# Performance work log

Measured on AMD Instinct MI355X. Metric: run time of the kernel, lower is better.

## Reference

```python
import jax, jax.numpy as jnp
import numpy as np

L = 16            # table_num (levels)
LOG2T = 14
T = 1 << LOG2T    # entries per table
Z = 512           # z_dim
S = 256           # style_dim
IMG = 256         # img_size
RES_MIN, RES_MAX = 16, 256
HID, OUT = 64, 3  # mlp hidden / out dims
B = 8
FDIM = 2 * L      # retrieved feature dim (2 per level)
PRIME = jnp.uint32(2654435761)  # instant-ngp hash prime
GAIN = 1.4142135623730951       # stylegan lrelu gain sqrt(2)
# geometric level resolutions res_min -> res_max
RES = np.floor(RES_MIN * np.exp(np.arange(L) * np.log(RES_MAX / RES_MIN) / (L - 1))).astype(np.float32)


def _lrelu(x):
    return GAIN * jnp.where(x >= 0, x, 0.2 * x)


def _coords():
    c = (jnp.arange(IMG, dtype=jnp.float32) + 0.5) / IMG
    x, y = jnp.meshgrid(c, c, indexing='ij')
    return jnp.stack((x, y), -1).reshape(-1, 2)  # (N, 2), N = IMG*IMG


def _mod_linear(x, s, aw, ab, w, b):
    # StyleGAN2-style modulated linear with demodulation. x: (B,N,in), s: (B,S)
    style = s @ aw + ab                                   # (B, in)
    demod = jax.lax.rsqrt((style ** 2) @ (w ** 2) + 1e-8)  # (B, out)
    return ((x * style[:, None, :]) @ w) * demod[:, None, :] + b


def _forward(z, mw0, mb0, mw1, mb1, mw2, mb2, base_tables, w_mod, b_mod,
             a0w, a0b, w0, bb0, a1w, a1b, w1, bb1, a2w, a2b, w2, bb2):
    s = _lrelu(z @ mw0 + mb0)
    s = _lrelu(s @ mw1 + mb1)
    s = _lrelu(s @ mw2 + mb2)                              # (B, S)
    # style-conditioned hash tables: per-level per-channel modulation of base tables
    scale = 1.0 + (s @ w_mod + b_mod).reshape(-1, L, 1, 2)
    tables = base_tables[None] * scale                     # (B, L, T, 2)

    coords = _coords()                                     # (N, 2)
    offs = jnp.array([[0, 0], [1, 0], [0, 1], [1, 1]], dtype=jnp.uint32)
    feats = []
    for l in range(L):
        pos = coords * RES[l]
        p0 = jnp.floor(pos)
        frac = pos - p0                                    # (N, 2)
        p0i = p0.astype(jnp.uint32)
        cx = p0i[None, :, 0] + offs[:, 0:1]                # (4, N)
        cy = p0i[None, :, 1] + offs[:, 1:2]
        idx = ((cx ^ (cy * PRIME)) & jnp.uint32(T - 1)).astype(jnp.int32)  # (4, N)
        wx = jnp.where(offs[:, 0:1] == 1, frac[None, :, 0], 1.0 - frac[None, :, 0])
        wy = jnp.where(offs[:, 1:2] == 1, frac[None, :, 1], 1.0 - frac[None, :, 1])
        wgt = wx * wy                                      # (4, N)
        tl = tables[:, l]                                  # (B, T, 2)
        f = jnp.take(tl, idx.reshape(-1), axis=1).reshape(tl.shape[0], 4, -1, 2)
        feats.append(jnp.einsum('bcnd,cn->bnd', f, wgt))   # bilinear interp
    h = jnp.concatenate(feats, -1)                         # (B, N, 2L)

    # stacked modulated MLP (3 layers), final tanh, then render to image
    h = _lrelu(_mod_linear(h, s, a0w, a0b, w0, bb0))
    h = _lrelu(_mod_linear(h, s, a1w, a1b, w1, bb1))
    h = jnp.tanh(_mod_linear(h, s, a2w, a2b, w2, bb2))     # (B, N, 3)
    return h.reshape(-1, IMG, IMG, OUT).transpose(0, 3, 1, 2)


def setup_inputs() -> dict:
    key = jax.random.key(0)
    ks = jax.random.split(key, 12)
    nrm = lambda k, sh, sc: jax.random.normal(k, sh, jnp.float32) * sc
    inp = {}
    inp['z'] = jax.random.normal(ks[0], (B, Z), jnp.float32)
    inp['mw0'] = nrm(ks[1], (Z, S), 1 / np.sqrt(Z)); inp['mb0'] = jnp.zeros((S,), jnp.float32)
    inp['mw1'] = nrm(ks[2], (S, S), 1 / np.sqrt(S)); inp['mb1'] = jnp.zeros((S,), jnp.float32)
    inp['mw2'] = nrm(ks[3], (S, S), 1 / np.sqrt(S)); inp['mb2'] = jnp.zeros((S,), jnp.float32)
    inp['base_tables'] = nrm(ks[4], (L, T, 2), 0.1)
    inp['w_mod'] = nrm(ks[5], (S, L * 2), 1 / np.sqrt(S)); inp['b_mod'] = jnp.zeros((L * 2,), jnp.float32)
    inp['a0w'] = nrm(ks[6], (S, FDIM), 1 / np.sqrt(S)); inp['a0b'] = jnp.ones((FDIM,), jnp.float32)
    inp['w0'] = nrm(ks[7], (FDIM, HID), 1 / np.sqrt(FDIM)); inp['bb0'] = jnp.zeros((HID,), jnp.float32)
    inp['a1w'] = nrm(ks[8], (S, HID), 1 / np.sqrt(S)); inp['a1b'] = jnp.ones((HID,), jnp.float32)
    inp['w1'] = nrm(ks[9], (HID, HID), 1 / np.sqrt(HID)); inp['bb1'] = jnp.zeros((HID,), jnp.float32)
    inp['a2w'] = nrm(ks[10], (S, HID), 1 / np.sqrt(S)); inp['a2b'] = jnp.ones((HID,), jnp.float32)
    inp['w2'] = nrm(ks[11], (HID, OUT), 1 / np.sqrt(HID)); inp['bb2'] = jnp.zeros((OUT,), jnp.float32)
    return inp


def reference(z, mw0, mb0, mw1, mb1, mw2, mb2, base_tables, w_mod, b_mod,
              a0w, a0b, w0, bb0, a1w, a1b, w1, bb1, a2w, a2b, w2, bb2):
    return _forward(z, mw0, mb0, mw1, mb1, mw2, mb2, base_tables, w_mod, b_mod,
                    a0w, a0b, w0, bb0, a1w, a1b, w1, bb1, a2w, a2b, w2, bb2)
```

## Files before the change

### kernel.cpp

```cpp
#include <hip/hip_runtime.h>
#include <hip/hip_bf16.h>

#define NLVL 16
#define TSZ  16384
#define NB   8

typedef _Float16 h8 __attribute__((ext_vector_type(8)));
typedef float    f4 __attribute__((ext_vector_type(4)));

#define MFMA16(A,B,C) __builtin_amdgcn_mfma_f32_16x16x32_f16(A,B,C,0,0,0)
#define GAINF 1.41421356237309515f

__device__ const float RES_TAB[16] = {
  16.f, 19.f, 23.f, 27.f, 33.f, 40.f, 48.f, 58.f,
  70.f, 84.f, 101.f, 122.f, 147.f, 176.f, 212.f, 255.f
};

__device__ __forceinline__ float lrelu(float x) {
  float v = x < 0.0f ? 0.2f * x : x;
  return GAINF * v;
}
__device__ __forceinline__ float act(float x) { return fmaxf(x, 0.2f * x); }

__device__ __forceinline__ float tanh_fast(float x) {
  float t = __builtin_amdgcn_exp2f(x * 2.8853900817779268f);
  return 1.0f - 2.0f * __builtin_amdgcn_rcpf(t + 1.0f);
}

__device__ __forceinline__ unsigned pk(float a, float b) {
  union { decltype(__builtin_amdgcn_cvt_pkrtz(0.f, 0.f)) h; unsigned u; } U;
  U.h = __builtin_amdgcn_cvt_pkrtz(a, b);
  return U.u;
}
__device__ __forceinline__ unsigned pk_rne(float a, float b) {
  union { _Float16 h[2]; unsigned u; } U;
  U.h[0] = (_Float16)a; U.h[1] = (_Float16)b;
  return U.u;
}

__device__ __forceinline__ void hash4(const float* __restrict__ bt,
                                      int n, int l0, float* g8)
{
  const float inv = 1.0f / 256.0f;
  float cx = ((n >> 8) + 0.5f) * inv;
  float cy = ((n & 255) + 0.5f) * inv;
#pragma unroll
  for (int j = 0; j < 4; ++j) {
    float res = RES_TAB[l0 + j];
    float px = cx * res, py = cy * res;
    float fx0 = floorf(px), fy0 = floorf(py);
    float fx = px - fx0, fy = py - fy0;
    unsigned x0 = (unsigned)fx0, y0 = (unsigned)fy0;
    unsigned hy0 = y0 * 2654435761u;
    unsigned hy1 = (y0 + 1u) * 2654435761u;
    unsigned i00 = (x0 ^ hy0) & 16383u;
    unsigned i10 = ((x0 + 1u) ^ hy0) & 16383u;
    unsigned i01 = (x0 ^ hy1) & 16383u;
    unsigned i11 = ((x0 + 1u) ^ hy1) & 16383u;
    const float2* tb = (const float2*)(bt + (size_t)(l0 + j) * (TSZ * 2));
    float2 f00 = tb[i00], f10 = tb[i10], f01 = tb[i01], f11 = tb[i11];
    float wx0 = 1.0f - fx, wy0 = 1.0f - fy;
    float w00 = wx0 * wy0, w10 = fx * wy0, w01 = wx0 * fy, w11 = fx * fy;
    g8[2 * j]     = w00 * f00.x + w10 * f10.x + w01 * f01.x + w11 * f11.x;
    g8[2 * j + 1] = w00 * f00.y + w10 * f10.y + w01 * f01.y + w11 * f11.y;
  }
}
__device__ __forceinline__ void hash_features(const float* __restrict__ bt,
                                              int n, float* g)
{
#pragma unroll
  for (int q = 0; q < 4; ++q) hash4(bt, n, q * 4, g + 8 * q);
}

__device__ __forceinline__ void map_layer(const float* __restrict__ xs_in,
                                          float* __restrict__ out_lds,
                                          const float* __restrict__ W,
                                          const float* __restrict__ bias,
                                          int K, int t,
                                          float* __restrict__ part)
{
  const int j4 = (t & 63) * 4;
  const int ks = t >> 6;
  const int chunk = K >> 4;
  const int kb = ks * chunk;
  f4 a0 = {0,0,0,0}, a1 = {0,0,0,0}, a2 = {0,0,0,0}, a3 = {0,0,0,0};
  for (int k0 = 0; k0 < chunk; k0 += 16) {
    f4 wr[16];
#pragma unroll
    for (int u = 0; u < 16; ++u)
      wr[u] = *(const f4*)&W[(kb + k0 + u) * 256 + j4];
    float xr[16];
#pragma unroll
    for (int u = 0; u < 16; ++u) xr[u] = xs_in[kb + k0 + u];
#pragma unroll
    for (int u = 0; u < 16; u += 4) {
      a0 += xr[u + 0] * wr[u + 0];
      a1 += xr[u + 1] * wr[u + 1];
      a2 += xr[u + 2] * wr[u + 2];
      a3 += xr[u + 3] * wr[u + 3];
    }
  }
  *(f4*)&part[ks * 256 + j4] = (a0 + a1) + (a2 + a3);
  __syncthreads();
  if (t < 256) {
    float v = 0.f;
#pragma unroll
    for (int q = 0; q < 16; ++q) v += part[q * 256 + t];
    out_lds[t] = lrelu(bias[t] + v);
  }
  __syncthreads();
}

__global__ void __launch_bounds__(1024) k_pre(
    const float* __restrict__ z,
    const float* __restrict__ mw0, const float* __restrict__ mb0,
    const float* __restrict__ mw1, const float* __restrict__ mb1,
    const float* __restrict__ mw2, const float* __restrict__ mb2,
    const float* __restrict__ bt,
    const float* __restrict__ w_mod, const float* __restrict__ b_mod,
    const float* __restrict__ a0w, const float* __restrict__ a0b,
    const float* __restrict__ w0,
    const float* __restrict__ a1w, const float* __restrict__ a1b,
    const float* __restrict__ w1,
    const float* __restrict__ a2w, const float* __restrict__ a2b,
    const float* __restrict__ w2,
    _Float16* __restrict__ W0h, _Float16* __restrict__ W1h,
    _Float16* __restrict__ W2h, _Float16* __restrict__ ghf)
{
  __shared__ __align__(16) unsigned smem[16384];

  const int t = threadIdx.x;

  if (blockIdx.x >= 8) {
    const int hb  = blockIdx.x - 8;
    const int lvl = hb & 15;
    const int pg  = hb >> 4;
    const int gg  = lvl >> 2;
    const int sub = 2 * (lvl & 3);

    const float4* tb4 = (const float4*)(bt + (size_t)lvl * (TSZ * 2));
#pragma unroll
    for (int i = 0; i < 8; ++i) {
      float4 v = tb4[i * 1024 + t];
      int e = (i * 1024 + t) * 2;
      smem[e]     = pk_rne(v.x, v.y);
      smem[e + 1] = pk_rne(v.z, v.w);
    }
    __syncthreads();

    const int y = t & 255, xsub = t >> 8;
    const float res = RES_TAB[lvl];
    const float inv = 1.0f / 256.0f;
    float cy = (y + 0.5f) * inv;
    float py = cy * res;
    float fy0 = floorf(py);
    float fy = py - fy0;
    unsigned y0 = (unsigned)fy0;
    unsigned hy0 = y0 * 2654435761u;
    unsigned hy1 = (y0 + 1u) * 2654435761u;
    float wy0 = 1.0f - fy;
    const int cc = y & 15, th = y >> 4;

#pragma unroll
    for (int i = 0; i < 8; ++i) {
      int xo = xsub * 8 + i;
      float cx = (pg * 32 + xo + 0.5f) * inv;
      float px = cx * res;
      float fx0 = floorf(px);
      float fx = px - fx0;
      unsigned x0 = (unsigned)fx0;
      unsigned i00 = (x0 ^ hy0) & 16383u;
      unsigned i10 = ((x0 + 1u) ^ hy0) & 16383u;
      unsigned i01 = (x0 ^ hy1) & 16383u;
      unsigned i11 = ((x0 + 1u) ^ hy1) & 16383u;
      union { unsigned u; _Float16 h[2]; } e00, e10, e01, e11;
      e00.u = smem[i00]; e10.u = smem[i10];
      e01.u = smem[i01]; e11.u = smem[i11];
      float wx0 = 1.0f - fx;
      float w00 = wx0 * wy0, w10 = fx * wy0, w01 = wx0 * fy, w11 = fx * fy;
      float gx = w00 * (float)e00.h[0] + w10 * (float)e10.h[0]
               + w01 * (float)e01.h[0] + w11 * (float)e11.h[0];
      float gy = w00 * (float)e00.h[1] + w10 * (float)e10.h[1]
               + w01 * (float)e01.h[1] + w11 * (float)e11.h[1];
      int tile = pg * 512 + xo * 16 + th;
      *(unsigned*)&ghf[(size_t)tile * 512 + (gg * 16 + cc) * 8 + sub] =
          pk_rne(gx, gy);
    }
    return;
  }

  float* F    = (float*)smem;
  float* xs   = F;
  float* sA   = F + 512;
  float* sB   = F + 768;
  float* st0  = F + 1024;
  float* scf  = F + 1056;
  float* st1  = F + 1088;
  float* st2  = F + 1152;
  float* dm0  = F + 1216;
  float* dm1  = F + 1280;
  float* dm2  = F + 1344;
  float* part = F + 2048;

  const int b = blockIdx.x;

  if (t < 512) xs[t] = z[b * 512 + t];
  __syncthreads();

  map_layer(xs, sA, mw0, mb0, 512, t, part);
  map_layer(sA, sB, mw1, mb1, 256, t, part);
  map_layer(sB, xs, mw2, mb2, 256, t, part);
  const float* ss = xs;

  {
    const int jg = (t & 7) * 4, kc = t >> 3, kb = kc * 2;
    f4 wm0 = *(const f4*)&w_mod[(kb + 0) * 32 + jg];
    f4 wm1 = *(const f4*)&w_mod[(kb + 1) * 32 + jg];
    f4 aw0 = *(const f4*)&a0w[(kb + 0) * 32 + jg];
    f4 aw1 = *(const f4*)&a0w[(kb + 1) * 32 + jg];
    float s0 = ss[kb], s1 = ss[kb + 1];
    f4 am = s0 * wm0 + s1 * wm1;
    f4 as = s0 * aw0 + s1 * aw1;
    *(f4*)&part[kc * 32 + jg] = am;
    *(f4*)&part[4096 + kc * 32 + jg] = as;
  }
  __syncthreads();
  if (t < 32) {
    float am = b_mod[t], as = a0b[t];
#pragma unroll
    for (int q = 0; q < 128; ++q) { am += part[q * 32 + t]; as += part[4096 + q * 32 + t]; }
    scf[t] = 1.0f + am; st0[t] = as;
  }
  __syncthreads();

  {
    const int jg = (t & 15) * 4, kc = t >> 4, kb = kc * 4;
    f4 w1r[4], w2r[4];
#pragma unroll
    for (int k = 0; k < 4; ++k) w1r[k] = *(const f4*)&a1w[(kb + k) * 64 + jg];
#pragma unroll
    for (int k = 0; k < 4; ++k) w2r[k] = *(const f4*)&a2w[(kb + k) * 64 + jg];
    f4 v1 = {0,0,0,0}, v2 = {0,0,0,0};
#pragma unroll
    for (int k = 0; k < 4; ++k) {
      float sv = ss[kb + k];
      v1 += sv * w1r[k]; v2 += sv * w2r[k];
    }
    *(f4*)&part[kc * 64 + jg] = v1;
    *(f4*)&part[4096 + kc * 64 + jg] = v2;
  }
  __syncthreads();
  if (t >= 128 && t < 192) {
    int j = t - 128;
    float v1 = a1b[j], v2 = a2b[j];
#pragma unroll
    for (int q = 0; q < 64; ++q) { v1 += part[q * 64 + j]; v2 += part[4096 + q * 64 + j]; }
    st1[j] = v1; st2[j] = v2;
  }
  __syncthreads();

  if (t < 256) {
    int j = t & 63, q = t >> 6;
    float wv[8];
#pragma unroll
    for (int i = 0; i < 8; ++i) wv[i] = w0[(q * 8 + i) * 64 + j];
    float acc = (q == 0) ? 1e-8f : 0.f;
#pragma unroll
    for (int i = 0; i < 8; ++i) {
      float p = st0[q * 8 + i] * wv[i]; acc = fmaf(p, p, acc);
    }
    part[t] = acc;
  } else if (t < 768) {
    int u = t - 256, j = u & 63, q = u >> 6;
    float wv[8];
#pragma unroll
    for (int k = 0; k < 8; ++k) wv[k] = w1[(q * 8 + k) * 64 + j];
    float acc = (q == 0) ? 1e-8f : 0.f;
#pragma unroll
    for (int k = 0; k < 8; ++k) {
      float p = st1[q * 8 + k] * wv[k]; acc = fmaf(p, p, acc);
    }
    part[512 + u] = acc;
  } else if (t < 832) {
    int u = t - 768, ch = u & 3, q = u >> 2;
    if (ch < 3) {
      float wv[4];
#pragma unroll
      for (int k = 0; k < 4; ++k) wv[k] = w2[(q * 4 + k) * 3 + ch];
      float acc = (q == 0) ? 1e-8f : 0.f;
#pragma unroll
      for (int k = 0; k < 4; ++k) {
        float p = st2[q * 4 + k] * wv[k]; acc = fmaf(p, p, acc);
      }
      part[1024 + u] = acc;
    }
  }
  __syncthreads();
  if (t < 64) {
    float a = part[t] + part[64 + t] + part[128 + t] + part[192 + t];
    dm0[t] = 1.0f / sqrtf(a);
  } else if (t < 128) {
    int j = t - 64; float a = 0.f;
#pragma unroll
    for (int q = 0; q < 8; ++q) a += part[512 + q * 64 + j];
    dm1[j] = 1.0f / sqrtf(a);
  } else if (t >= 192 && t < 195) {
    int ch = t - 192; float a = 0.f;
#pragma unroll
    for (int q = 0; q < 16; ++q) a += part[1024 + q * 4 + ch];
    dm2[ch] = 1.0f / sqrtf(a);
  }
  __syncthreads();

  for (int f = t; f < 2048; f += 1024) {
    int j = f >> 5, i = f & 31;
    W0h[b * 2048 + f] = (_Float16)(scf[i] * st0[i] * w0[i * 64 + j] * dm0[j]);
  }
  for (int f = t; f < 4096; f += 1024) {
    int j2 = f >> 6, k = f & 63;
    W1h[b * 4096 + f] = (_Float16)(GAINF * st1[k] * w1[k * 64 + j2] * dm1[j2]);
  }
  {
    int f = t, ch = f >> 6, k = f & 63;
    if (f < 1024)
      W2h[b * 1024 + f] = (ch < 3) ? (_Float16)(GAINF * st2[k] * w2[k * 3 + ch] * dm2[ch])
                                   : (_Float16)0.0f;
  }
}

__device__ __forceinline__ void st4(_Float16* L, int pix, int jb, f4 v) {
  int ks = jb ^ ((pix & 7) << 3);
  union { unsigned u[2]; uint2 v2; } U;
  U.u[0] = pk(v[0], v[1]); U.u[1] = pk(v[2], v[3]);
  *(uint2*)(L + pix * 64 + ks) = U.v2;
}
__device__ __forceinline__ h8 ldf(const _Float16* L, int pix, int kb) {
  int ks = kb ^ ((pix & 7) << 3);
  return *(const h8*)(L + pix * 64 + ks);
}

template <int FUSED>
__global__ void __launch_bounds__(256) k_mlp(
    const _Float16* __restrict__ W0h, const _Float16* __restrict__ W1h,
    const _Float16* __restrict__ W2h, const _Float16* __restrict__ ghf,
    const float* __restrict__ bt,
    const float* __restrict__ bb0, const float* __restrict__ bb1,
    const float* __restrict__ bb2, float* __restrict__ out)
{
  __shared__ _Float16 lds[4][4096];
  __shared__ _Float16 hb[FUSED ? 8192 : 8];

  const int t = threadIdx.x;
  const int w = t >> 6, lane = t & 63;
  const int c = lane & 15, g = lane >> 4;
  const int b = blockIdx.y;
  const int pixb = blockIdx.x * 256 + w * 64;
  const int tile0 = pixb >> 4;
  _Float16* L = lds[w];

  if constexpr (FUSED) {
    float gl[32];
    hash_features(bt, blockIdx.x * 256 + t, gl);
    int tl = t >> 4, cl = t & 15;
#pragma unroll
    for (int gg = 0; gg < 4; ++gg) {
      union { unsigned u[4]; uint4 v; } U;
      U.u[0] = pk(gl[8 * gg + 0], gl[8 * gg + 1]);
      U.u[1] = pk(gl[8 * gg + 2], gl[8 * gg + 3]);
      U.u[2] = pk(gl[8 * gg + 4], gl[8 * gg + 5]);
      U.u[3] = pk(gl[8 * gg + 6], gl[8 * gg + 7]);
      *(uint4*)&hb[tl * 512 + (gg * 16 + cl) * 8] = U.v;
    }
    __syncthreads();
  }

  h8 A0[4], A1[4][2], A2[2];
#pragma unroll
  for (int jt = 0; jt < 4; ++jt)
    A0[jt] = *(const h8*)&W0h[b * 2048 + (jt * 16 + c) * 32 + 8 * g];
#pragma unroll
  for (int jt = 0; jt < 4; ++jt)
#pragma unroll
    for (int kf = 0; kf < 2; ++kf)
      A1[jt][kf] = *(const h8*)&W1h[b * 4096 + (jt * 16 + c) * 64 + kf * 32 + 8 * g];
#pragma unroll
  for (int kf = 0; kf < 2; ++kf)
    A2[kf] = *(const h8*)&W2h[b * 1024 + c * 64 + kf * 32 + 8 * g];

  f4 bv0[4], bv1[4], bv2;
#pragma unroll
  for (int jt = 0; jt < 4; ++jt) {
    bv0[jt] = *(const f4*)&bb0[jt * 16 + 4 * g];
    bv1[jt] = *(const f4*)&bb1[jt * 16 + 4 * g];
  }
  if (g == 0) { bv2 = f4{bb2[0], bb2[1], bb2[2], 0.0f}; }
  else        { bv2 = f4{0.0f, 0.0f, 0.0f, 0.0f}; }

  f4 acc[4][4];
#pragma unroll
  for (int pt = 0; pt < 4; ++pt) {
    h8 Bh;
    if constexpr (FUSED) {
      Bh = *(const h8*)&hb[(w * 4 + pt) * 512 + lane * 8];
    } else {
      Bh = *(const h8*)&ghf[(size_t)(tile0 + pt) * 512 + lane * 8];
    }
#pragma unroll
    for (int jt = 0; jt < 4; ++jt)
      acc[jt][pt] = MFMA16(A0[jt], Bh, bv0[jt]);
  }

#pragma unroll
  for (int jt = 0; jt < 4; ++jt)
#pragma unroll
    for (int pt = 0; pt < 4; ++pt) {
      f4 v = acc[jt][pt];
#pragma unroll
      for (int r = 0; r < 4; ++r) v[r] = act(v[r]);
      st4(L, pt * 16 + c, jt * 16 + 4 * g, v);
    }

  f4 acc1[4][4];
#pragma unroll
  for (int pt = 0; pt < 4; ++pt) {
    h8 Bf0 = ldf(L, pt * 16 + c, 0 * 32 + 8 * g);
    h8 Bf1 = ldf(L, pt * 16 + c, 1 * 32 + 8 * g);
#pragma unroll
    for (int jt = 0; jt < 4; ++jt) {
      f4 a = MFMA16(A1[jt][0], Bf0, bv1[jt]);
      acc1[jt][pt] = MFMA16(A1[jt][1], Bf1, a);
    }
  }

#pragma unroll
  for (int jt = 0; jt < 4; ++jt)
#pragma unroll
    for (int pt = 0; pt < 4; ++pt) {
      f4 v = acc1[jt][pt];
#pragma unroll
      for (int r = 0; r < 4; ++r) v[r] = act(v[r]);
      st4(L, pt * 16 + c, jt * 16 + 4 * g, v);
    }

#pragma unroll
  for (int pt = 0; pt < 4; ++pt) {
    h8 Bf0 = ldf(L, pt * 16 + c, 0 * 32 + 8 * g);
    h8 Bf1 = ldf(L, pt * 16 + c, 1 * 32 + 8 * g);
    f4 a = MFMA16(A2[0], Bf0, bv2);
    a = MFMA16(A2[1], Bf1, a);
    if (g == 0) {
      int pix = pixb + pt * 16 + c;
#pragma unroll
      for (int r = 0; r < 3; ++r)
        out[((b * 3 + r) << 16) + pix] = tanh_fast(a[r]);
    }
  }
}

extern "C" void kernel_launch(void* const* d_in, const int* in_sizes, int n_in,
                              void* d_out, int out_size, void* d_ws, size_t ws_size,
                              hipStream_t stream)
{
  const float* z    = (const float*)d_in[0];
  const float* mw0  = (const float*)d_in[1];
  const float* mb0  = (const float*)d_in[2];
  const float* mw1  = (const float*)d_in[3];
  const float* mb1  = (const float*)d_in[4];
  const float* mw2  = (const float*)d_in[5];
  const float* mb2  = (const float*)d_in[6];
  const float* bt   = (const float*)d_in[7];
  const float* wmod = (const float*)d_in[8];
  const float* bmod = (const float*)d_in[9];
  const float* a0w  = (const float*)d_in[10];
  const float* a0b  = (const float*)d_in[11];
  const float* w0   = (const float*)d_in[12];
  const float* bb0  = (const float*)d_in[13];
  const float* a1w  = (const float*)d_in[14];
  const float* a1b  = (const float*)d_in[15];
  const float* w1   = (const float*)d_in[16];
  const float* bb1  = (const float*)d_in[17];
  const float* a2w  = (const float*)d_in[18];
  const float* a2b  = (const float*)d_in[19];
  const float* w2   = (const float*)d_in[20];
  const float* bb2  = (const float*)d_in[21];

  char* ws = (char*)d_ws;
  _Float16* W0h = (_Float16*)(ws);
  _Float16* W1h = (_Float16*)(ws + 32768);
  _Float16* W2h = (_Float16*)(ws + 98304);
  _Float16* ghf = (_Float16*)(ws + 114688);
  float* out = (float*)d_out;

  if (ws_size >= (size_t)4308992) {
    k_pre<<<8 + 128, 1024, 0, stream>>>(z, mw0, mb0, mw1, mb1, mw2, mb2, bt,
                                        wmod, bmod, a0w, a0b, w0,
                                        a1w, a1b, w1, a2w, a2b, w2,
                                        W0h, W1h, W2h, ghf);
    k_mlp<0><<<dim3(256, NB), 256, 0, stream>>>(W0h, W1h, W2h, ghf, bt,
                                                bb0, bb1, bb2, out);
  } else {
    k_pre<<<8, 1024, 0, stream>>>(z, mw0, mb0, mw1, mb1, mw2, mb2, bt,
                                  wmod, bmod, a0w, a0b, w0,
                                  a1w, a1b, w1, a2w, a2b, w2,
                                  W0h, W1h, W2h, ghf);
    k_mlp<1><<<dim3(256, NB), 256, 0, stream>>>(W0h, W1h, W2h, ghf, bt,
                                                bb0, bb1, bb2, out);
  }
}
```

Baseline: 44.30 us.

## Split style mapping into multi-block kernels with split-K partial sums

Replaces the single per-batch 8-block preprocessing kernel, which ran the three mapping FC layers serially inside 8 workgroups, with a chain of kernels: layer 0 fused with the hash-grid precompute, two split-K layer kernels over 128 blocks, a style projection kernel, and a fold kernel that builds the fp16 modulated weights. Partial sums go through workspace buffers and are reduced by the next kernel. This is meant to spread the latency-bound weight reads across many more CUs, at the cost of extra launches and global round trips. The fallback path gets a separate style-only kernel with lightly restructured demod loops.

```diff
diff --git a/kernel.cpp b/kernel.cpp
--- a/kernel.cpp
+++ b/kernel.cpp
@@ -72,67 +72,16 @@
   for (int q = 0; q < 4; ++q) hash4(bt, n, q * 4, g + 8 * q);
 }
 
-__device__ __forceinline__ void map_layer(const float* __restrict__ xs_in,
-                                          float* __restrict__ out_lds,
-                                          const float* __restrict__ W,
-                                          const float* __restrict__ bias,
-                                          int K, int t,
-                                          float* __restrict__ part)
-{
-  const int j4 = (t & 63) * 4;
-  const int ks = t >> 6;
-  const int chunk = K >> 4;
-  const int kb = ks * chunk;
-  f4 a0 = {0,0,0,0}, a1 = {0,0,0,0}, a2 = {0,0,0,0}, a3 = {0,0,0,0};
-  for (int k0 = 0; k0 < chunk; k0 += 16) {
-    f4 wr[16];
-#pragma unroll
-    for (int u = 0; u < 16; ++u)
-      wr[u] = *(const f4*)&W[(kb + k0 + u) * 256 + j4];
-    float xr[16];
-#pragma unroll
-    for (int u = 0; u < 16; ++u) xr[u] = xs_in[kb + k0 + u];
-#pragma unroll
-    for (int u = 0; u < 16; u += 4) {
-      a0 += xr[u + 0] * wr[u + 0];
-      a1 += xr[u + 1] * wr[u + 1];
-      a2 += xr[u + 2] * wr[u + 2];
-      a3 += xr[u + 3] * wr[u + 3];
-    }
-  }
-  *(f4*)&part[ks * 256 + j4] = (a0 + a1) + (a2 + a3);
-  __syncthreads();
-  if (t < 256) {
-    float v = 0.f;
-#pragma unroll
-    for (int q = 0; q < 16; ++q) v += part[q * 256 + t];
-    out_lds[t] = lrelu(bias[t] + v);
-  }
-  __syncthreads();
-}
-
-__global__ void __launch_bounds__(1024) k_pre(
-    const float* __restrict__ z,
-    const float* __restrict__ mw0, const float* __restrict__ mb0,
-    const float* __restrict__ mw1, const float* __restrict__ mb1,
-    const float* __restrict__ mw2, const float* __restrict__ mb2,
+__global__ void __launch_bounds__(1024) k_l0h(
+    const float* __restrict__ z, const float* __restrict__ mw0,
     const float* __restrict__ bt,
-    const float* __restrict__ w_mod, const float* __restrict__ b_mod,
-    const float* __restrict__ a0w, const float* __restrict__ a0b,
-    const float* __restrict__ w0,
-    const float* __restrict__ a1w, const float* __restrict__ a1b,
-    const float* __restrict__ w1,
-    const float* __restrict__ a2w, const float* __restrict__ a2b,
-    const float* __restrict__ w2,
-    _Float16* __restrict__ W0h, _Float16* __restrict__ W1h,
-    _Float16* __restrict__ W2h, _Float16* __restrict__ ghf)
+    float* __restrict__ pA, _Float16* __restrict__ ghf)
 {
   __shared__ __align__(16) unsigned smem[16384];
-
   const int t = threadIdx.x;
 
-  if (blockIdx.x >= 8) {
-    const int hb  = blockIdx.x - 8;
+  if (blockIdx.x >= 128) {
+    const int hb  = blockIdx.x - 128;
     const int lvl = hb & 15;
     const int pg  = hb >> 4;
     const int gg  = lvl >> 2;
@@ -189,7 +138,251 @@
     return;
   }
 
-  float* F    = (float*)smem;
+  float* part = (float*)smem;
+  const int b = blockIdx.x >> 4, ks = blockIdx.x & 15;
+  const int j = t & 255, ksub = t >> 8;
+  const int kb = ks * 32 + ksub * 8;
+  float acc = 0.f;
+#pragma unroll
+  for (int u = 0; u < 8; ++u)
+    acc = fmaf(z[b * 512 + kb + u], mw0[(kb + u) * 256 + j], acc);
+  part[ksub * 256 + j] = acc;
+  __syncthreads();
+  if (t < 256)
+    pA[(b * 16 + ks) * 256 + t] =
+        part[t] + part[256 + t] + part[512 + t] + part[768 + t];
+}
+
+__global__ void __launch_bounds__(1024) k_layer(
+    const float* __restrict__ pin, const float* __restrict__ bias,
+    const float* __restrict__ W, float* __restrict__ pout)
+{
+  __shared__ float xs[256];
+  __shared__ float part[1024];
+  const int t = threadIdx.x;
+  const int b = blockIdx.x >> 4, ks = blockIdx.x & 15;
+  if (t < 256) {
+    float v = bias[t];
+#pragma unroll
+    for (int q = 0; q < 16; ++q) v += pin[(b * 16 + q) * 256 + t];
+    xs[t] = lrelu(v);
+  }
+  __syncthreads();
+  const int j = t & 255, ksub = t >> 8;
+  const int kb = ks * 16 + ksub * 4;
+  float acc = 0.f;
+#pragma unroll
+  for (int u = 0; u < 4; ++u)
+    acc = fmaf(xs[kb + u], W[(kb + u) * 256 + j], acc);
+  part[ksub * 256 + j] = acc;
+  __syncthreads();
+  if (t < 256)
+    pout[(b * 16 + ks) * 256 + t] =
+        part[t] + part[256 + t] + part[512 + t] + part[768 + t];
+}
+
+__global__ void __launch_bounds__(1024) k_proj(
+    const float* __restrict__ pin, const float* __restrict__ mb2,
+    const float* __restrict__ w_mod, const float* __restrict__ b_mod,
+    const float* __restrict__ a0w, const float* __restrict__ a0b,
+    const float* __restrict__ a1w, const float* __restrict__ a1b,
+    const float* __restrict__ a2w, const float* __restrict__ a2b,
+    float* __restrict__ stws)
+{
+  __shared__ float ss[256];
+  __shared__ float part[2048];
+  const int t = threadIdx.x;
+  const int b = blockIdx.x / 3, sec = blockIdx.x % 3;
+  if (t < 256) {
+    float v = mb2[t];
+#pragma unroll
+    for (int q = 0; q < 16; ++q) v += pin[(b * 16 + q) * 256 + t];
+    ss[t] = lrelu(v);
+  }
+  __syncthreads();
+  float* sw = stws + b * 192;
+  if (sec == 0) {
+    int j = t & 31, kc = t >> 5;
+    float am = 0.f, as = 0.f;
+#pragma unroll
+    for (int u = 0; u < 8; ++u) {
+      float sv = ss[kc * 8 + u];
+      am = fmaf(sv, w_mod[(kc * 8 + u) * 32 + j], am);
+      as = fmaf(sv, a0w[(kc * 8 + u) * 32 + j], as);
+    }
+    part[t] = am; part[1024 + t] = as;
+    __syncthreads();
+    if (t < 32) {
+      float am2 = b_mod[t], as2 = a0b[t];
+#pragma unroll
+      for (int q = 0; q < 32; ++q) {
+        am2 += part[q * 32 + t]; as2 += part[1024 + q * 32 + t];
+      }
+      sw[t] = as2;
+      sw[32 + t] = 1.0f + am2;
+    }
+  } else {
+    const float* aw = (sec == 1) ? a1w : a2w;
+    const float* ab = (sec == 1) ? a1b : a2b;
+    int j = t & 63, kc = t >> 6;
+    float v = 0.f;
+#pragma unroll
+    for (int u = 0; u < 16; ++u)
+      v = fmaf(ss[kc * 16 + u], aw[(kc * 16 + u) * 64 + j], v);
+    part[t] = v;
+    __syncthreads();
+    if (t < 64) {
+      float v2 = ab[t];
+#pragma unroll
+      for (int q = 0; q < 16; ++q) v2 += part[q * 64 + t];
+      sw[(sec == 1 ? 64 : 128) + t] = v2;
+    }
+  }
+}
+
+__global__ void __launch_bounds__(1024) k_fold(
+    const float* __restrict__ stws,
+    const float* __restrict__ w0, const float* __restrict__ w1,
+    const float* __restrict__ w2,
+    _Float16* __restrict__ W0h, _Float16* __restrict__ W1h,
+    _Float16* __restrict__ W2h)
+{
+  __shared__ float st0[32], scf[32], st1[64], st2[64];
+  __shared__ float dm0[64], dm1[64], dm2[4];
+  __shared__ float part[1088];
+  const int t = threadIdx.x;
+  const int b = blockIdx.x;
+  const float* sw = stws + b * 192;
+  if (t < 32) { st0[t] = sw[t]; scf[t] = sw[32 + t]; }
+  else if (t >= 64 && t < 128)  st1[t - 64]  = sw[t];
+  else if (t >= 128 && t < 192) st2[t - 128] = sw[t];
+  __syncthreads();
+
+  if (t < 256) {
+    int j = t & 63, q = t >> 6;
+    float wv[8];
+#pragma unroll
+    for (int i = 0; i < 8; ++i) wv[i] = w0[(q * 8 + i) * 64 + j];
+    float acc = (q == 0) ? 1e-8f : 0.f;
+#pragma unroll
+    for (int i = 0; i < 8; ++i) {
+      float p = st0[q * 8 + i] * wv[i]; acc = fmaf(p, p, acc);
+    }
+    part[t] = acc;
+  } else if (t < 768) {
+    int u = t - 256, j = u & 63, q = u >> 6;
+    float wv[8];
+#pragma unroll
+    for (int k = 0; k < 8; ++k) wv[k] = w1[(q * 8 + k) * 64 + j];
+    float acc = (q == 0) ? 1e-8f : 0.f;
+#pragma unroll
+    for (int k = 0; k < 8; ++k) {
+      float p = st1[q * 8 + k] * wv[k]; acc = fmaf(p, p, acc);
+    }
+    part[512 + u] = acc;
+  } else if (t < 832) {
+    int u = t - 768, ch = u & 3, q = u >> 2;
+    if (ch < 3) {
+      float wv[4];
+#pragma unroll
+      for (int k = 0; k < 4; ++k) wv[k] = w2[(q * 4 + k) * 3 + ch];
+      float acc = (q == 0) ? 1e-8f : 0.f;
+#pragma unroll
+      for (int k = 0; k < 4; ++k) {
+        float p = st2[q * 4 + k] * wv[k]; acc = fmaf(p, p, acc);
+      }
+      part[1024 + u] = acc;
+    }
+  }
+  __syncthreads();
+  if (t < 64) {
+    float a = part[t] + part[64 + t] + part[128 + t] + part[192 + t];
+    dm0[t] = 1.0f / sqrtf(a);
+  } else if (t < 128) {
+    int j = t - 64; float a = 0.f;
+#pragma unroll
+    for (int q = 0; q < 8; ++q) a += part[512 + q * 64 + j];
+    dm1[j] = 1.0f / sqrtf(a);
+  } else if (t >= 192 && t < 195) {
+    int ch = t - 192; float a = 0.f;
+#pragma unroll
+    for (int q = 0; q < 16; ++q) a += part[1024 + q * 4 + ch];
+    dm2[ch] = 1.0f / sqrtf(a);
+  }
+  __syncthreads();
+
+  for (int f = t; f < 2048; f += 1024) {
+    int j = f >> 5, i = f & 31;
+    W0h[b * 2048 + f] = (_Float16)(scf[i] * st0[i] * w0[i * 64 + j] * dm0[j]);
+  }
+  for (int f = t; f < 4096; f += 1024) {
+    int j2 = f >> 6, k = f & 63;
+    W1h[b * 4096 + f] = (_Float16)(GAINF * st1[k] * w1[k * 64 + j2] * dm1[j2]);
+  }
+  {
+    int f = t, ch = f >> 6, k = f & 63;
+    if (f < 1024)
+      W2h[b * 1024 + f] = (ch < 3)
+          ? (_Float16)(GAINF * st2[k] * w2[k * 3 + ch] * dm2[ch])
+          : (_Float16)0.0f;
+  }
+}
+
+__device__ __forceinline__ void map_layer(const float* __restrict__ xs_in,
+                                          float* __restrict__ out_lds,
+                                          const float* __restrict__ W,
+                                          const float* __restrict__ bias,
+                                          int K, int t,
+                                          float* __restrict__ part)
+{
+  const int j4 = (t & 63) * 4;
+  const int ks = t >> 6;
+  const int chunk = K >> 4;
+  const int kb = ks * chunk;
+  f4 a0 = {0,0,0,0}, a1 = {0,0,0,0}, a2 = {0,0,0,0}, a3 = {0,0,0,0};
+  for (int k0 = 0; k0 < chunk; k0 += 16) {
+    f4 wr[16];
+#pragma unroll
+    for (int u = 0; u < 16; ++u)
+      wr[u] = *(const f4*)&W[(kb + k0 + u) * 256 + j4];
+    float xr[16];
+#pragma unroll
+    for (int u = 0; u < 16; ++u) xr[u] = xs_in[kb + k0 + u];
+#pragma unroll
+    for (int u = 0; u < 16; u += 4) {
+      a0 += xr[u + 0] * wr[u + 0];
+      a1 += xr[u + 1] * wr[u + 1];
+      a2 += xr[u + 2] * wr[u + 2];
+      a3 += xr[u + 3] * wr[u + 3];
+    }
+  }
+  *(f4*)&part[ks * 256 + j4] = (a0 + a1) + (a2 + a3);
+  __syncthreads();
+  if (t < 256) {
+    float v = 0.f;
+#pragma unroll
+    for (int q = 0; q < 16; ++q) v += part[q * 256 + t];
+    out_lds[t] = lrelu(bias[t] + v);
+  }
+  __syncthreads();
+}
+
+__global__ void __launch_bounds__(1024) k_style1(
+    const float* __restrict__ z,
+    const float* __restrict__ mw0, const float* __restrict__ mb0,
+    const float* __restrict__ mw1, const float* __restrict__ mb1,
+    const float* __restrict__ mw2, const float* __restrict__ mb2,
+    const float* __restrict__ w_mod, const float* __restrict__ b_mod,
+    const float* __restrict__ a0w, const float* __restrict__ a0b,
+    const float* __restrict__ w0,
+    const float* __restrict__ a1w, const float* __restrict__ a1b,
+    const float* __restrict__ w1,
+    const float* __restrict__ a2w, const float* __restrict__ a2b,
+    const float* __restrict__ w2,
+    _Float16* __restrict__ W0h, _Float16* __restrict__ W1h,
+    _Float16* __restrict__ W2h)
+{
+  __shared__ __align__(16) float F[10240];
   float* xs   = F;
   float* sA   = F + 512;
   float* sB   = F + 768;
@@ -201,12 +394,11 @@
   float* dm1  = F + 1280;
   float* dm2  = F + 1344;
   float* part = F + 2048;
-
+  const int t = threadIdx.x;
   const int b = blockIdx.x;
 
   if (t < 512) xs[t] = z[b * 512 + t];
   __syncthreads();
-
   map_layer(xs, sA, mw0, mb0, 512, t, part);
   map_layer(sA, sB, mw1, mb1, 256, t, part);
   map_layer(sB, xs, mw2, mb2, 256, t, part);
@@ -232,7 +424,6 @@
     scf[t] = 1.0f + am; st0[t] = as;
   }
   __syncthreads();
-
   {
     const int jg = (t & 15) * 4, kc = t >> 4, kb = kc * 4;
     f4 w1r[4], w2r[4];
@@ -258,39 +449,29 @@
     st1[j] = v1; st2[j] = v2;
   }
   __syncthreads();
-
   if (t < 256) {
     int j = t & 63, q = t >> 6;
-    float wv[8];
-#pragma unroll
-    for (int i = 0; i < 8; ++i) wv[i] = w0[(q * 8 + i) * 64 + j];
     float acc = (q == 0) ? 1e-8f : 0.f;
 #pragma unroll
-    for (int i = 0; i < 8; ++i) {
-      float p = st0[q * 8 + i] * wv[i]; acc = fmaf(p, p, acc);
+    for (int i = q * 8; i < q * 8 + 8; ++i) {
+      float p = st0[i] * w0[i * 64 + j]; acc = fmaf(p, p, acc);
     }
     part[t] = acc;
   } else if (t < 768) {
     int u = t - 256, j = u & 63, q = u >> 6;
-    float wv[8];
-#pragma unroll
-    for (int k = 0; k < 8; ++k) wv[k] = w1[(q * 8 + k) * 64 + j];
     float acc = (q == 0) ? 1e-8f : 0.f;
 #pragma unroll
-    for (int k = 0; k < 8; ++k) {
-      float p = st1[q * 8 + k] * wv[k]; acc = fmaf(p, p, acc);
+    for (int k = q * 8; k < q * 8 + 8; ++k) {
+      float p = st1[k] * w1[k * 64 + j]; acc = fmaf(p, p, acc);
     }
     part[512 + u] = acc;
   } else if (t < 832) {
     int u = t - 768, ch = u & 3, q = u >> 2;
     if (ch < 3) {
-      float wv[4];
-#pragma unroll
-      for (int k = 0; k < 4; ++k) wv[k] = w2[(q * 4 + k) * 3 + ch];
       float acc = (q == 0) ? 1e-8f : 0.f;
 #pragma unroll
-      for (int k = 0; k < 4; ++k) {
-        float p = st2[q * 4 + k] * wv[k]; acc = fmaf(p, p, acc);
+      for (int k = q * 4; k < q * 4 + 4; ++k) {
+        float p = st2[k] * w2[k * 3 + ch]; acc = fmaf(p, p, acc);
       }
       part[1024 + u] = acc;
     }
@@ -311,7 +492,6 @@
     dm2[ch] = 1.0f / sqrtf(a);
   }
   __syncthreads();
-
   for (int f = t; f < 2048; f += 1024) {
     int j = f >> 5, i = f & 31;
     W0h[b * 2048 + f] = (_Float16)(scf[i] * st0[i] * w0[i * 64 + j] * dm0[j]);
@@ -489,20 +669,25 @@
   _Float16* W1h = (_Float16*)(ws + 32768);
   _Float16* W2h = (_Float16*)(ws + 98304);
   _Float16* ghf = (_Float16*)(ws + 114688);
+  float*    pA  = (float*)(ws + 4308992);
+  float*    pB  = (float*)(ws + 4440064);
+  float*    stw = (float*)(ws + 4571136);
   float* out = (float*)d_out;
 
-  if (ws_size >= (size_t)4308992) {
-    k_pre<<<8 + 128, 1024, 0, stream>>>(z, mw0, mb0, mw1, mb1, mw2, mb2, bt,
-                                        wmod, bmod, a0w, a0b, w0,
-                                        a1w, a1b, w1, a2w, a2b, w2,
-                                        W0h, W1h, W2h, ghf);
+  if (ws_size >= (size_t)4577280) {
+    k_l0h<<<256, 1024, 0, stream>>>(z, mw0, bt, pA, ghf);
+    k_layer<<<128, 1024, 0, stream>>>(pA, mb0, mw1, pB);
+    k_layer<<<128, 1024, 0, stream>>>(pB, mb1, mw2, pA);
+    k_proj<<<24, 1024, 0, stream>>>(pA, mb2, wmod, bmod, a0w, a0b,
+                                    a1w, a1b, a2w, a2b, stw);
+    k_fold<<<NB, 1024, 0, stream>>>(stw, w0, w1, w2, W0h, W1h, W2h);
     k_mlp<0><<<dim3(256, NB), 256, 0, stream>>>(W0h, W1h, W2h, ghf, bt,
                                                 bb0, bb1, bb2, out);
   } else {
-    k_pre<<<8, 1024, 0, stream>>>(z, mw0, mb0, mw1, mb1, mw2, mb2, bt,
-                                  wmod, bmod, a0w, a0b, w0,
-                                  a1w, a1b, w1, a2w, a2b, w2,
-                                  W0h, W1h, W2h, ghf);
+    k_style1<<<NB, 1024, 0, stream>>>(z, mw0, mb0, mw1, mb1, mw2, mb2,
+                                      wmod, bmod, a0w, a0b, w0,
+                                      a1w, a1b, w1, a2w, a2b, w2,
+                                      W0h, W1h, W2h);
     k_mlp<1><<<dim3(256, NB), 256, 0, stream>>>(W0h, W1h, W2h, ghf, bt,
                                                 bb0, bb1, bb2, out);
   }
```

New measurement: 44.27 us. No clear change (-0.1%).

## Split serial style mapping into multi-block kernels and planarize hash feature layout

Applied to the files above, without the earlier changes.

The single k_pre kernel ran the 3-layer mapping MLP, the style projections and the weight folding in only 8 blocks, one per batch element, which left most of the GPU idle. This splits that work into a chain of kernels (layer 0 fused with hash precompute, two layer kernels, a projection kernel, a fold kernel). Each layer kernel splits K across 16 blocks per batch and writes partial sums that the next kernel reduces. The hash features are now stored as per-level planes and gathered into MFMA fragments with four strided loads instead of one vectorized load. The cost is several extra kernel launches and dependency hops, plus less coalesced feature loads in the MLP.

```diff
diff --git a/kernel.cpp b/kernel.cpp
--- a/kernel.cpp
+++ b/kernel.cpp
@@ -72,71 +72,18 @@
   for (int q = 0; q < 4; ++q) hash4(bt, n, q * 4, g + 8 * q);
 }
 
-__device__ __forceinline__ void map_layer(const float* __restrict__ xs_in,
-                                          float* __restrict__ out_lds,
-                                          const float* __restrict__ W,
-                                          const float* __restrict__ bias,
-                                          int K, int t,
-                                          float* __restrict__ part)
-{
-  const int j4 = (t & 63) * 4;
-  const int ks = t >> 6;
-  const int chunk = K >> 4;
-  const int kb = ks * chunk;
-  f4 a0 = {0,0,0,0}, a1 = {0,0,0,0}, a2 = {0,0,0,0}, a3 = {0,0,0,0};
-  for (int k0 = 0; k0 < chunk; k0 += 16) {
-    f4 wr[16];
-#pragma unroll
-    for (int u = 0; u < 16; ++u)
-      wr[u] = *(const f4*)&W[(kb + k0 + u) * 256 + j4];
-    float xr[16];
-#pragma unroll
-    for (int u = 0; u < 16; ++u) xr[u] = xs_in[kb + k0 + u];
-#pragma unroll
-    for (int u = 0; u < 16; u += 4) {
-      a0 += xr[u + 0] * wr[u + 0];
-      a1 += xr[u + 1] * wr[u + 1];
-      a2 += xr[u + 2] * wr[u + 2];
-      a3 += xr[u + 3] * wr[u + 3];
-    }
-  }
-  *(f4*)&part[ks * 256 + j4] = (a0 + a1) + (a2 + a3);
-  __syncthreads();
-  if (t < 256) {
-    float v = 0.f;
-#pragma unroll
-    for (int q = 0; q < 16; ++q) v += part[q * 256 + t];
-    out_lds[t] = lrelu(bias[t] + v);
-  }
-  __syncthreads();
-}
-
-__global__ void __launch_bounds__(1024) k_pre(
-    const float* __restrict__ z,
-    const float* __restrict__ mw0, const float* __restrict__ mb0,
-    const float* __restrict__ mw1, const float* __restrict__ mb1,
-    const float* __restrict__ mw2, const float* __restrict__ mb2,
+__global__ void __launch_bounds__(1024) k_l0h(
+    const float* __restrict__ z, const float* __restrict__ mw0,
     const float* __restrict__ bt,
-    const float* __restrict__ w_mod, const float* __restrict__ b_mod,
-    const float* __restrict__ a0w, const float* __restrict__ a0b,
-    const float* __restrict__ w0,
-    const float* __restrict__ a1w, const float* __restrict__ a1b,
-    const float* __restrict__ w1,
-    const float* __restrict__ a2w, const float* __restrict__ a2b,
-    const float* __restrict__ w2,
-    _Float16* __restrict__ W0h, _Float16* __restrict__ W1h,
-    _Float16* __restrict__ W2h, _Float16* __restrict__ ghf)
+    float* __restrict__ pA, unsigned* __restrict__ ghfp)
 {
   __shared__ __align__(16) unsigned smem[16384];
-
   const int t = threadIdx.x;
 
-  if (blockIdx.x >= 8) {
-    const int hb  = blockIdx.x - 8;
+  if (blockIdx.x >= 128) {
+    const int hb  = blockIdx.x - 128;
     const int lvl = hb & 15;
     const int pg  = hb >> 4;
-    const int gg  = lvl >> 2;
-    const int sub = 2 * (lvl & 3);
 
     const float4* tb4 = (const float4*)(bt + (size_t)lvl * (TSZ * 2));
 #pragma unroll
@@ -159,8 +106,8 @@
     unsigned hy0 = y0 * 2654435761u;
     unsigned hy1 = (y0 + 1u) * 2654435761u;
     float wy0 = 1.0f - fy;
-    const int cc = y & 15, th = y >> 4;
-
+
+    unsigned* plane = ghfp + (size_t)lvl * 65536;
 #pragma unroll
     for (int i = 0; i < 8; ++i) {
       int xo = xsub * 8 + i;
@@ -182,81 +129,129 @@
                + w01 * (float)e01.h[0] + w11 * (float)e11.h[0];
       float gy = w00 * (float)e00.h[1] + w10 * (float)e10.h[1]
                + w01 * (float)e01.h[1] + w11 * (float)e11.h[1];
-      int tile = pg * 512 + xo * 16 + th;
-      *(unsigned*)&ghf[(size_t)tile * 512 + (gg * 16 + cc) * 8 + sub] =
-          pk_rne(gx, gy);
+      plane[(pg * 32 + xo) * 256 + y] = pk_rne(gx, gy);
     }
     return;
   }
 
-  float* F    = (float*)smem;
-  float* xs   = F;
-  float* sA   = F + 512;
-  float* sB   = F + 768;
-  float* st0  = F + 1024;
-  float* scf  = F + 1056;
-  float* st1  = F + 1088;
-  float* st2  = F + 1152;
-  float* dm0  = F + 1216;
-  float* dm1  = F + 1280;
-  float* dm2  = F + 1344;
-  float* part = F + 2048;
-
+  float* part = (float*)smem;
+  const int b = blockIdx.x >> 4, ks = blockIdx.x & 15;
+  const int j = t & 255, ksub = t >> 8;
+  const int kb = ks * 32 + ksub * 8;
+  float acc = 0.f;
+#pragma unroll
+  for (int u = 0; u < 8; ++u)
+    acc = fmaf(z[b * 512 + kb + u], mw0[(kb + u) * 256 + j], acc);
+  part[ksub * 256 + j] = acc;
+  __syncthreads();
+  if (t < 256)
+    pA[(b * 16 + ks) * 256 + t] =
+        part[t] + part[256 + t] + part[512 + t] + part[768 + t];
+}
+
+__global__ void __launch_bounds__(1024) k_layer(
+    const float* __restrict__ pin, const float* __restrict__ bias,
+    const float* __restrict__ W, float* __restrict__ pout)
+{
+  __shared__ float xs[256];
+  __shared__ float part[1024];
+  const int t = threadIdx.x;
+  const int b = blockIdx.x >> 4, ks = blockIdx.x & 15;
+  if (t < 256) {
+    float v = bias[t];
+#pragma unroll
+    for (int q = 0; q < 16; ++q) v += pin[(b * 16 + q) * 256 + t];
+    xs[t] = lrelu(v);
+  }
+  __syncthreads();
+  const int j = t & 255, ksub = t >> 8;
+  const int kb = ks * 16 + ksub * 4;
+  float acc = 0.f;
+#pragma unroll
+  for (int u = 0; u < 4; ++u)
+    acc = fmaf(xs[kb + u], W[(kb + u) * 256 + j], acc);
+  part[ksub * 256 + j] = acc;
+  __syncthreads();
+  if (t < 256)
+    pout[(b * 16 + ks) * 256 + t] =
+        part[t] + part[256 + t] + part[512 + t] + part[768 + t];
+}
+
+__global__ void __launch_bounds__(1024) k_proj(
+    const float* __restrict__ pin, const float* __restrict__ mb2,
+    const float* __restrict__ w_mod, const float* __restrict__ b_mod,
+    const float* __restrict__ a0w, const float* __restrict__ a0b,
+    const float* __restrict__ a1w, const float* __restrict__ a1b,
+    const float* __restrict__ a2w, const float* __restrict__ a2b,
+    float* __restrict__ stws)
+{
+  __shared__ float ss[256];
+  __shared__ float part[2048];
+  const int t = threadIdx.x;
+  const int b = blockIdx.x / 3, sec = blockIdx.x % 3;
+  if (t < 256) {
+    float v = mb2[t];
+#pragma unroll
+    for (int q = 0; q < 16; ++q) v += pin[(b * 16 + q) * 256 + t];
+    ss[t] = lrelu(v);
+  }
+  __syncthreads();
+  float* sw = stws + b * 192;
+  if (sec == 0) {
+    int j = t & 31, kc = t >> 5;
+    float am = 0.f, as = 0.f;
+#pragma unroll
+    for (int u = 0; u < 8; ++u) {
+      float sv = ss[kc * 8 + u];
+      am = fmaf(sv, w_mod[(kc * 8 + u) * 32 + j], am);
+      as = fmaf(sv, a0w[(kc * 8 + u) * 32 + j], as);
+    }
+    part[t] = am; part[1024 + t] = as;
+    __syncthreads();
+    if (t < 32) {
+      float am2 = b_mod[t], as2 = a0b[t];
+#pragma unroll
+      for (int q = 0; q < 32; ++q) {
+        am2 += part[q * 32 + t]; as2 += part[1024 + q * 32 + t];
+      }
+      sw[t] = as2;
+      sw[32 + t] = 1.0f + am2;
+    }
+  } else {
+    const float* aw = (sec == 1) ? a1w : a2w;
+    const float* ab = (sec == 1) ? a1b : a2b;
+    int j = t & 63, kc = t >> 6;
+    float v = 0.f;
+#pragma unroll
+    for (int u = 0; u < 16; ++u)
+      v = fmaf(ss[kc * 16 + u], aw[(kc * 16 + u) * 64 + j], v);
+    part[t] = v;
+    __syncthreads();
+    if (t < 64) {
+      float v2 = ab[t];
+#pragma unroll
+      for (int q = 0; q < 16; ++q) v2 += part[q * 64 + t];
+      sw[(sec == 1 ? 64 : 128) + t] = v2;
+    }
+  }
+}
+
+__global__ void __launch_bounds__(1024) k_fold(
+    const float* __restrict__ stws,
+    const float* __restrict__ w0, const float* __restrict__ w1,
+    const float* __restrict__ w2,
+    _Float16* __restrict__ W0h, _Float16* __restrict__ W1h,
+    _Float16* __restrict__ W2h)
+{
+  __shared__ float st0[32], scf[32], st1[64], st2[64];
+  __shared__ float dm0[64], dm1[64], dm2[4];
+  __shared__ float part[1088];
+  const int t = threadIdx.x;
   const int b = blockIdx.x;
-
-  if (t < 512) xs[t] = z[b * 512 + t];
-  __syncthreads();
-
-  map_layer(xs, sA, mw0, mb0, 512, t, part);
-  map_layer(sA, sB, mw1, mb1, 256, t, part);
-  map_layer(sB, xs, mw2, mb2, 256, t, part);
-  const float* ss = xs;
-
-  {
-    const int jg = (t & 7) * 4, kc = t >> 3, kb = kc * 2;
-    f4 wm0 = *(const f4*)&w_mod[(kb + 0) * 32 + jg];
-    f4 wm1 = *(const f4*)&w_mod[(kb + 1) * 32 + jg];
-    f4 aw0 = *(const f4*)&a0w[(kb + 0) * 32 + jg];
-    f4 aw1 = *(const f4*)&a0w[(kb + 1) * 32 + jg];
-    float s0 = ss[kb], s1 = ss[kb + 1];
-    f4 am = s0 * wm0 + s1 * wm1;
-    f4 as = s0 * aw0 + s1 * aw1;
-    *(f4*)&part[kc * 32 + jg] = am;
-    *(f4*)&part[4096 + kc * 32 + jg] = as;
-  }
-  __syncthreads();
-  if (t < 32) {
-    float am = b_mod[t], as = a0b[t];
-#pragma unroll
-    for (int q = 0; q < 128; ++q) { am += part[q * 32 + t]; as += part[4096 + q * 32 + t]; }
-    scf[t] = 1.0f + am; st0[t] = as;
-  }
-  __syncthreads();
-
-  {
-    const int jg = (t & 15) * 4, kc = t >> 4, kb = kc * 4;
-    f4 w1r[4], w2r[4];
-#pragma unroll
-    for (int k = 0; k < 4; ++k) w1r[k] = *(const f4*)&a1w[(kb + k) * 64 + jg];
-#pragma unroll
-    for (int k = 0; k < 4; ++k) w2r[k] = *(const f4*)&a2w[(kb + k) * 64 + jg];
-    f4 v1 = {0,0,0,0}, v2 = {0,0,0,0};
-#pragma unroll
-    for (int k = 0; k < 4; ++k) {
-      float sv = ss[kb + k];
-      v1 += sv * w1r[k]; v2 += sv * w2r[k];
-    }
-    *(f4*)&part[kc * 64 + jg] = v1;
-    *(f4*)&part[4096 + kc * 64 + jg] = v2;
-  }
-  __syncthreads();
-  if (t >= 128 && t < 192) {
-    int j = t - 128;
-    float v1 = a1b[j], v2 = a2b[j];
-#pragma unroll
-    for (int q = 0; q < 64; ++q) { v1 += part[q * 64 + j]; v2 += part[4096 + q * 64 + j]; }
-    st1[j] = v1; st2[j] = v2;
-  }
+  const float* sw = stws + b * 192;
+  if (t < 32) { st0[t] = sw[t]; scf[t] = sw[32 + t]; }
+  else if (t >= 64 && t < 128)  st1[t - 64]  = sw[t];
+  else if (t >= 128 && t < 192) st2[t - 128] = sw[t];
   __syncthreads();
 
   if (t < 256) {
@@ -323,8 +318,9 @@
   {
     int f = t, ch = f >> 6, k = f & 63;
     if (f < 1024)
-      W2h[b * 1024 + f] = (ch < 3) ? (_Float16)(GAINF * st2[k] * w2[k * 3 + ch] * dm2[ch])
-                                   : (_Float16)0.0f;
+      W2h[b * 1024 + f] = (ch < 3)
+          ? (_Float16)(GAINF * st2[k] * w2[k * 3 + ch] * dm2[ch])
+          : (_Float16)0.0f;
   }
 }
 
@@ -342,7 +338,7 @@
 template <int FUSED>
 __global__ void __launch_bounds__(256) k_mlp(
     const _Float16* __restrict__ W0h, const _Float16* __restrict__ W1h,
-    const _Float16* __restrict__ W2h, const _Float16* __restrict__ ghf,
+    const _Float16* __restrict__ W2h, const unsigned* __restrict__ ghfp,
     const float* __restrict__ bt,
     const float* __restrict__ bb0, const float* __restrict__ bb1,
     const float* __restrict__ bb2, float* __restrict__ out)
@@ -403,7 +399,12 @@
     if constexpr (FUSED) {
       Bh = *(const h8*)&hb[(w * 4 + pt) * 512 + lane * 8];
     } else {
-      Bh = *(const h8*)&ghf[(size_t)(tile0 + pt) * 512 + lane * 8];
+      int px = (tile0 + pt) * 16 + c;
+      union { unsigned u[4]; h8 h; } B;
+#pragma unroll
+      for (int j = 0; j < 4; ++j)
+        B.u[j] = ghfp[(size_t)(4 * g + j) * 65536 + px];
+      Bh = B.h;
     }
 #pragma unroll
     for (int jt = 0; jt < 4; ++jt)
@@ -485,25 +486,32 @@
   const float* bb2  = (const float*)d_in[21];
 
   char* ws = (char*)d_ws;
-  _Float16* W0h = (_Float16*)(ws);
-  _Float16* W1h = (_Float16*)(ws + 32768);
-  _Float16* W2h = (_Float16*)(ws + 98304);
-  _Float16* ghf = (_Float16*)(ws + 114688);
+  _Float16* W0h  = (_Float16*)(ws);
+  _Float16* W1h  = (_Float16*)(ws + 32768);
+  _Float16* W2h  = (_Float16*)(ws + 98304);
+  unsigned* ghfp = (unsigned*)(ws + 114688);
+  float*    pA   = (float*)(ws + 4308992);
+  float*    pB   = (float*)(ws + 4440064);
+  float*    stw  = (float*)(ws + 4571136);
   float* out = (float*)d_out;
 
-  if (ws_size >= (size_t)4308992) {
-    k_pre<<<8 + 128, 1024, 0, stream>>>(z, mw0, mb0, mw1, mb1, mw2, mb2, bt,
-                                        wmod, bmod, a0w, a0b, w0,
-                                        a1w, a1b, w1, a2w, a2b, w2,
-                                        W0h, W1h, W2h, ghf);
-    k_mlp<0><<<dim3(256, NB), 256, 0, stream>>>(W0h, W1h, W2h, ghf, bt,
+  if (ws_size >= (size_t)4577280) {
+    k_l0h<<<256, 1024, 0, stream>>>(z, mw0, bt, pA, ghfp);
+    k_layer<<<128, 1024, 0, stream>>>(pA, mb0, mw1, pB);
+    k_layer<<<128, 1024, 0, stream>>>(pB, mb1, mw2, pA);
+    k_proj<<<24, 1024, 0, stream>>>(pA, mb2, wmod, bmod, a0w, a0b,
+                                    a1w, a1b, a2w, a2b, stw);
+    k_fold<<<NB, 1024, 0, stream>>>(stw, w0, w1, w2, W0h, W1h, W2h);
+    k_mlp<0><<<dim3(256, NB), 256, 0, stream>>>(W0h, W1h, W2h, ghfp, bt,
                                                 bb0, bb1, bb2, out);
   } else {
-    k_pre<<<8, 1024, 0, stream>>>(z, mw0, mb0, mw1, mb1, mw2, mb2, bt,
-                                  wmod, bmod, a0w, a0b, w0,
-                                  a1w, a1b, w1, a2w, a2b, w2,
-                                  W0h, W1h, W2h, ghf);
-    k_mlp<1><<<dim3(256, NB), 256, 0, stream>>>(W0h, W1h, W2h, ghf, bt,
+    k_l0h<<<128, 1024, 0, stream>>>(z, mw0, bt, pA, ghfp);
+    k_layer<<<128, 1024, 0, stream>>>(pA, mb0, mw1, pB);
+    k_layer<<<128, 1024, 0, stream>>>(pB, mb1, mw2, pA);
+    k_proj<<<24, 1024, 0, stream>>>(pA, mb2, wmod, bmod, a0w, a0b,
+                                    a1w, a1b, a2w, a2b, stw);
+    k_fold<<<NB, 1024, 0, stream>>>(stw, w0, w1, w2, W0h, W1h, W2h);
+    k_mlp<1><<<dim3(256, NB), 256, 0, stream>>>(W0h, W1h, W2h, ghfp, bt,
                                                 bb0, bb1, bb2, out);
   }
 }
```

Measured after the change: 49.53 us. 1.12x slower.
